# Optimization experiments

Hardware: AMD Instinct MI355X
Metric: run time of the kernel (lower is better)

Reference implementation:

```python
import jax, jax.numpy as jnp
import numpy as np

T, H, F = 4096, 4096, 14336

def setup_inputs() -> dict:
    key = jax.random.key(0)
    k1, k2, k3, k4 = jax.random.split(key, 4)
    s = 1.0 / np.sqrt(H)
    return {
        "x": jax.random.normal(k1, (T, H), dtype=jnp.float32),
        "expert_w1": jax.random.normal(k2, (H, F), dtype=jnp.float32) * s,
        "expert_v1": jax.random.normal(k3, (H, F), dtype=jnp.float32) * s,
        "expert_w2": jax.random.normal(k4, (H, F), dtype=jnp.float32) * s,
    }

def reference(x, expert_w1, expert_v1, expert_w2):
    # SwiGLU expert FFN: silu(x @ w1) * (x @ v1) @ w2.T
    gate_proj = jax.nn.silu(x @ expert_w1)          # [T, F]
    up_proj = x @ expert_v1                          # [T, F]
    down_proj = (gate_proj * up_proj) @ expert_w2.T  # [T, H]
    return down_proj
```

## Files before the change

### kernel.cpp

```cpp
#include <hip/hip_runtime.h>
#include <hip/hip_bf16.h>
#include <stdint.h>

#define TT 4096
#define HH 4096
#define FF 14336
#define NCAT (2 * FF)

typedef __attribute__((ext_vector_type(8))) short bf16x8;
typedef __attribute__((ext_vector_type(4))) float f32x4;

__device__ __forceinline__ unsigned short f32_to_bf16(float f) {
    union { float f; unsigned int u; } v; v.f = f;
    unsigned int r = v.u + 0x7FFFu + ((v.u >> 16) & 1u);
    return (unsigned short)(r >> 16);
}

#define GLOAD16(g, l)                                                          \
    __builtin_amdgcn_global_load_lds(                                          \
        (const __attribute__((address_space(1))) void*)(g),                    \
        (__attribute__((address_space(3))) void*)(l), 16, 0, 0)

__global__ void cvt_lin(const float* __restrict__ in,
                        unsigned short* __restrict__ out, long n4) {
    long stride = (long)gridDim.x * blockDim.x;
    for (long i = (long)blockIdx.x * blockDim.x + threadIdx.x; i < n4; i += stride) {
        float4 v = *(const float4*)(in + i * 4);
        ushort4 o;
        o.x = f32_to_bf16(v.x); o.y = f32_to_bf16(v.y);
        o.z = f32_to_bf16(v.z); o.w = f32_to_bf16(v.w);
        *(ushort4*)(out + i * 4) = o;
    }
}

__global__ void cvt_tri(const float* __restrict__ in,
                        unsigned short* __restrict__ out, int off) {
    __shared__ float tile[64][65];
    int bh = blockIdx.x & 63;
    int bf = blockIdx.x >> 6;
    int t = threadIdx.x;
    int r16 = t >> 4;
    int c4 = (t & 15) * 4;
#pragma unroll
    for (int it = 0; it < 4; ++it) {
        int h = r16 + it * 16;
        float4 v = *(const float4*)(in + (size_t)(bh * 64 + h) * FF + bf * 64 + c4);
        tile[h][c4 + 0] = v.x; tile[h][c4 + 1] = v.y;
        tile[h][c4 + 2] = v.z; tile[h][c4 + 3] = v.w;
    }
    __syncthreads();
#pragma unroll
    for (int it = 0; it < 4; ++it) {
        int f = r16 + it * 16;
        int fg = bf * 64 + f;
        int row_out = ((fg >> 4) << 5) + (fg & 15) + off;
        ushort4 o;
        o.x = f32_to_bf16(tile[c4 + 0][f]);
        o.y = f32_to_bf16(tile[c4 + 1][f]);
        o.z = f32_to_bf16(tile[c4 + 2][f]);
        o.w = f32_to_bf16(tile[c4 + 3][f]);
        *(ushort4*)(out + (size_t)row_out * HH + bh * 64 + c4) = o;
    }
}


#define STG_A(BUF, SLOT, T) do {                                               \
    char* d_ = (char*)smem + (((BUF)*2 + (SLOT)) << 14) + tid * 16;            \
    GLOAD16(Abase + ((size_t)oA[SLOT] + (size_t)(T) * 128), d_);               \
    GLOAD16(Abase + ((size_t)oA[SLOT] + CA + (size_t)(T) * 128), d_ + 8192);   \
  } while (0)

#define STG_B(BUF, SLOT, T) do {                                               \
    char* d_ = (char*)smem + 65536 + (((BUF)*2 + (SLOT)) << 14) + tid * 16;    \
    GLOAD16(Bbase + ((size_t)oB[SLOT] + (size_t)(T) * 128), d_);               \
    GLOAD16(Bbase + ((size_t)oB[SLOT] + CB + (size_t)(T) * 128), d_ + 8192);   \
  } while (0)

#define READ_A(DST, BUF, MQ) do {                                              \
    const char* pA_ = (const char*)smem + (((BUF)*2 + (MQ)) << 14);            \
    _Pragma("unroll") for (int i_ = 0; i_ < 4; ++i_)                           \
    _Pragma("unroll") for (int k_ = 0; k_ < 2; ++k_)                           \
      DST[i_][k_] = *(const bf16x8*)(pA_ + ((((wr*64 + i_*16 + fr) << 7) + k_*64 + kg2) ^ lmask)); \
  } while (0)

#define READ_B(DST, BUF, NQ) do {                                              \
    const char* pB_ = (const char*)smem + 65536 + (((BUF)*2 + (NQ)) << 14);    \
    _Pragma("unroll") for (int j_ = 0; j_ < 2; ++j_)                           \
    _Pragma("unroll") for (int k_ = 0; k_ < 2; ++k_)                           \
      DST[j_][k_] = *(const bf16x8*)(pB_ + ((((wc*32 + j_*16 + fr) << 7) + k_*64 + kg2) ^ lmask)); \
  } while (0)

#define MFMA_Q(MQ, NQ, AF, BF)                                                 \
    _Pragma("unroll") for (int i_ = 0; i_ < 4; ++i_)                           \
    _Pragma("unroll") for (int j_ = 0; j_ < 2; ++j_)                           \
    _Pragma("unroll") for (int k_ = 0; k_ < 2; ++k_)                           \
      acc[MQ][i_][NQ][j_] = __builtin_amdgcn_mfma_f32_16x16x32_bf16(           \
          AF[i_][k_], BF[j_][k_], acc[MQ][i_][NQ][j_], 0, 0, 0)

#define BAR do {                                                               \
    asm volatile("" ::: "memory");                                             \
    __builtin_amdgcn_s_barrier();                                              \
    asm volatile("" ::: "memory");                                             \
  } while (0)

#define VMC8 asm volatile("s_waitcnt vmcnt(8)" ::: "memory")
#define VMC0 asm volatile("s_waitcnt vmcnt(0)" ::: "memory")

#define PHX(READS, STAGES, MQ, NQ, AF, BF, FENCE, POST) do {                   \
    READS;                                                                     \
    STAGES;                                                                    \
    __builtin_amdgcn_s_setprio(1);                                             \
    MFMA_Q(MQ, NQ, AF, BF);                                                    \
    __builtin_amdgcn_s_setprio(0);                                             \
    FENCE;                                                                     \
    POST;                                                                      \
    BAR;                                                                       \
  } while (0)

#define PH(READS, STAGES, MQ, NQ, AF, BF, FENCE)                               \
    PHX(READS, STAGES, MQ, NQ, AF, BF, FENCE, )

#define HALF_STG(BUF, OB, TS)                                                  \
    PH(READ_A(af, BUF, 0), , 0, 0, af, bfA, );                                 \
    PH(READ_B(bfB, BUF, 1), STG_A(BUF, 0, TS); STG_B(BUF, 0, TS), 0, 1, af, bfB, ); \
    PH(READ_A(af, BUF, 1), STG_B(BUF, 1, TS), 1, 1, af, bfB, );                \
    PHX(, STG_A(BUF, 1, TS), 1, 0, af, bfA, VMC8, READ_B(bfA, OB, 0));

#define HALF_T1(BUF, OB)                                                       \
    PH(READ_A(af, BUF, 0), , 0, 0, af, bfA, );                                 \
    PH(READ_B(bfB, BUF, 1), , 0, 1, af, bfB, );                                \
    PH(READ_A(af, BUF, 1), , 1, 1, af, bfB, );                                 \
    PHX(, , 1, 0, af, bfA, VMC0, READ_B(bfA, OB, 0));

#define HALF_T2(BUF)                                                           \
    PH(READ_A(af, BUF, 0), , 0, 0, af, bfA, );                                 \
    PH(READ_B(bfB, BUF, 1), , 0, 1, af, bfB, );                                \
    PH(READ_A(af, BUF, 1), , 1, 1, af, bfB, );                                 \
    PHX(, , 1, 0, af, bfA, , );

#define GEMM8_CORE(A_, LDA_, B_, LDB_, NT_)                                    \
  extern __shared__ char smem[];                                               \
  const char* const Abase = (const char*)(A_);                                 \
  const char* const Bbase = (const char*)(B_);                                 \
  const size_t CA = (size_t)(LDA_) * 256;                                      \
  const size_t CB = (size_t)(LDB_) * 256;                                      \
  const int tid = threadIdx.x;                                                 \
  const int lane = tid & 63;                                                   \
  const int wid = tid >> 6;                                                    \
  const int wr = wid >> 2;                                                     \
  const int wc = wid & 3;                                                      \
  const int fr = lane & 15;                                                    \
  const int kg2 = ((lane >> 4) & 3) << 4;                                      \
  const int lmask = (fr & 6) << 4;                                             \
  f32x4 acc[2][4][2][2];                                                       \
  _Pragma("unroll") for (int a_ = 0; a_ < 2; ++a_)                             \
  _Pragma("unroll") for (int b_ = 0; b_ < 4; ++b_)                             \
  _Pragma("unroll") for (int c_ = 0; c_ < 2; ++c_)                             \
  _Pragma("unroll") for (int d_ = 0; d_ < 2; ++d_)                             \
    acc[a_][b_][c_][d_] = (f32x4){0.f, 0.f, 0.f, 0.f};                         \
  bf16x8 af[4][2], bfA[2][2], bfB[2][2];                                       \
  unsigned int oA[2], oB[2];                                                   \
  {                                                                            \
    int d_ = tid * 16;                                                         \
    int p_ = d_ ^ (((d_ >> 8) & 3) << 5);                                      \
    int prow = p_ >> 7, pcol = (p_ & 127) >> 1;                                \
    _Pragma("unroll") for (int s_ = 0; s_ < 2; ++s_) {                         \
      int grA = m0 + s_ * 64 + (prow & 63);                                    \
      oA[s_] = (unsigned)((size_t)grA * (LDA_) + pcol) * 2u;                   \
      int grB = n0 + (prow >> 5) * 64 + s_ * 32 + (prow & 31);                 \
      oB[s_] = (unsigned)((size_t)grB * (LDB_) + pcol) * 2u;                   \
    }                                                                          \
  }                                                                            \
     \
  STG_A(0, 0, 0); STG_B(0, 0, 0); STG_B(0, 1, 0); STG_A(0, 1, 0);              \
  STG_A(1, 0, 1); STG_B(1, 0, 1); STG_B(1, 1, 1); STG_A(1, 1, 1);              \
  VMC8;                                                                        \
  __builtin_amdgcn_s_barrier();                                                \
  asm volatile("" ::: "memory");                                               \
  READ_B(bfA, 0, 0);                                                           \
  const int niter = (NT_) / 2;                                                 \
  for (int I = 0; I < niter - 1; ++I) {                                        \
    HALF_STG(0, 1, 2 * I + 2)                                                  \
    HALF_STG(1, 0, 2 * I + 3)                                                  \
  }                                                                            \
  HALF_T1(0, 1)                                                                \
  HALF_T2(1)

__global__ __launch_bounds__(512)
__attribute__((amdgpu_waves_per_eu(1, 2))) void gemm_swiglu(
    const unsigned short* __restrict__ Xb,
    const unsigned short* __restrict__ Wcat,
    unsigned short* __restrict__ Act) {
    int lid = blockIdx.x;
    const int m0 = (lid & 15) * 256;
    const int n0 = (lid >> 4) * 256;

    GEMM8_CORE(Xb, HH, Wcat, HH, HH / 64)

    const int dm = ((lane >> 4) & 3) * 4;
    const int dn = lane & 15;
#pragma unroll
    for (int mq = 0; mq < 2; ++mq)
#pragma unroll
        for (int i = 0; i < 4; ++i)
#pragma unroll
            for (int nq = 0; nq < 2; ++nq) {
                int rowb = m0 + wr * 128 + mq * 64 + i * 16 + dm;
                int col = (n0 + wc * 64 + nq * 32) / 2 + dn;
                f32x4 g4 = acc[mq][i][nq][0];
                f32x4 u4 = acc[mq][i][nq][1];
#pragma unroll
                for (int r = 0; r < 4; ++r) {
                    float g = g4[r], u = u4[r];
                    float s = g * u / (1.0f + __expf(-g));
                    Act[(size_t)(rowb + r) * FF + col] = f32_to_bf16(s);
                }
            }
}

__global__ __launch_bounds__(512)
__attribute__((amdgpu_waves_per_eu(1, 2))) void gemm_down(
    const unsigned short* __restrict__ Act,
    const unsigned short* __restrict__ W2b,
    float* __restrict__ Out) {
    int lid = blockIdx.x;
    const int m0 = (lid & 15) * 256;
    const int n0 = (lid >> 4) * 256;

    GEMM8_CORE(Act, FF, W2b, FF, FF / 64)

    const int dm = ((lane >> 4) & 3) * 4;
    const int dn = lane & 15;
#pragma unroll
    for (int mq = 0; mq < 2; ++mq)
#pragma unroll
        for (int i = 0; i < 4; ++i)
#pragma unroll
            for (int nq = 0; nq < 2; ++nq)
#pragma unroll
                for (int j = 0; j < 2; ++j) {
                    int rowb = m0 + wr * 128 + mq * 64 + i * 16 + dm;
                    int col = n0 + wc * 64 + nq * 32 + j * 16 + dn;
                    f32x4 v = acc[mq][i][nq][j];
#pragma unroll
                    for (int r = 0; r < 4; ++r)
                        Out[(size_t)(rowb + r) * HH + col] = v[r];
                }
}

extern "C" void kernel_launch(void* const* d_in, const int* in_sizes, int n_in,
                              void* d_out, int out_size, void* d_ws, size_t ws_size,
                              hipStream_t stream) {
    const float* x  = (const float*)d_in[0];
    const float* w1 = (const float*)d_in[1];
    const float* v1 = (const float*)d_in[2];
    const float* w2 = (const float*)d_in[3];
    float* out = (float*)d_out;

    unsigned short* xb   = (unsigned short*)d_ws;
    unsigned short* wcat = xb + (size_t)TT * HH;
    unsigned short* w2b  = wcat + (size_t)NCAT * HH;
    unsigned short* act  = w2b + (size_t)HH * FF;

    hipFuncSetAttribute((const void*)gemm_swiglu,
                        hipFuncAttributeMaxDynamicSharedMemorySize, 131072);
    hipFuncSetAttribute((const void*)gemm_down,
                        hipFuncAttributeMaxDynamicSharedMemorySize, 131072);

    cvt_lin<<<2048, 256, 0, stream>>>(x, xb, (long)TT * HH / 4);
    cvt_lin<<<2048, 256, 0, stream>>>(w2, w2b, (long)HH * FF / 4);
    cvt_tri<<<(HH / 64) * (FF / 64), 256, 0, stream>>>(w1, wcat, 0);
    cvt_tri<<<(HH / 64) * (FF / 64), 256, 0, stream>>>(v1, wcat, 16);

    gemm_swiglu<<<(TT / 256) * (NCAT / 256), 512, 131072, stream>>>(xb, wcat, act);
    gemm_down<<<(TT / 256) * (HH / 256), 512, 131072, stream>>>(act, w2b, out);
}
```

Baseline: 1.283 ms.

## Restructure GEMM main loop into two-phase k-steps with shifted staging

Replaces the four-phase-per-half pipeline, which had one barrier per quarter MFMA block, with a two-phase k-step. Each phase reads a larger set of LDS fragments, issues global-to-LDS stages for future tiles, then runs two MFMA quadrants before a single barrier. This halves the number of barriers per k-tile and reshuffles when the A/B stages for the next buffers are issued (the A second half is staged one tile ahead into the other buffer), so the prologue wait becomes vmcnt(6). It aims to cut sync overhead, but it risks LDS write/read hazards and less even overlap between loads and MFMA.

New measurement: 1.302 ms. Within noise of the previous version (+1.5%).

```diff
diff --git a/kernel.cpp b/kernel.cpp
--- a/kernel.cpp
+++ b/kernel.cpp
@@ -104,39 +104,58 @@
   } while (0)
 
 #define VMC8 asm volatile("s_waitcnt vmcnt(8)" ::: "memory")
+#define VMC6 asm volatile("s_waitcnt vmcnt(6)" ::: "memory")
 #define VMC0 asm volatile("s_waitcnt vmcnt(0)" ::: "memory")
 
-#define PHX(READS, STAGES, MQ, NQ, AF, BF, FENCE, POST) do {                   \
-    READS;                                                                     \
-    STAGES;                                                                    \
-    __builtin_amdgcn_s_setprio(1);                                             \
-    MFMA_Q(MQ, NQ, AF, BF);                                                    \
-    __builtin_amdgcn_s_setprio(0);                                             \
-    FENCE;                                                                     \
-    POST;                                                                      \
+#define KSTEP(BUF, OB, TAU)                                                    \
+    READ_A(af, BUF, 0);                                                        \
+    READ_B(bfA, BUF, 0);                                                       \
+    READ_B(bfB, BUF, 1);                                                       \
+    STG_A(OB, 1, (TAU) + 1);                                                   \
+    __builtin_amdgcn_s_setprio(1);                                             \
+    MFMA_Q(0, 0, af, bfA);                                                     \
+    MFMA_Q(0, 1, af, bfB);                                                     \
+    __builtin_amdgcn_s_setprio(0);                                             \
+    VMC8;                                                                      \
     BAR;                                                                       \
-  } while (0)
-
-#define PH(READS, STAGES, MQ, NQ, AF, BF, FENCE)                               \
-    PHX(READS, STAGES, MQ, NQ, AF, BF, FENCE, )
-
-#define HALF_STG(BUF, OB, TS)                                                  \
-    PH(READ_A(af, BUF, 0), , 0, 0, af, bfA, );                                 \
-    PH(READ_B(bfB, BUF, 1), STG_A(BUF, 0, TS); STG_B(BUF, 0, TS), 0, 1, af, bfB, ); \
-    PH(READ_A(af, BUF, 1), STG_B(BUF, 1, TS), 1, 1, af, bfB, );                \
-    PHX(, STG_A(BUF, 1, TS), 1, 0, af, bfA, VMC8, READ_B(bfA, OB, 0));
-
-#define HALF_T1(BUF, OB)                                                       \
-    PH(READ_A(af, BUF, 0), , 0, 0, af, bfA, );                                 \
-    PH(READ_B(bfB, BUF, 1), , 0, 1, af, bfB, );                                \
-    PH(READ_A(af, BUF, 1), , 1, 1, af, bfB, );                                 \
-    PHX(, , 1, 0, af, bfA, VMC0, READ_B(bfA, OB, 0));
-
-#define HALF_T2(BUF)                                                           \
-    PH(READ_A(af, BUF, 0), , 0, 0, af, bfA, );                                 \
-    PH(READ_B(bfB, BUF, 1), , 0, 1, af, bfB, );                                \
-    PH(READ_A(af, BUF, 1), , 1, 1, af, bfB, );                                 \
-    PHX(, , 1, 0, af, bfA, , );
+    READ_A(af, BUF, 1);                                                        \
+    STG_A(BUF, 0, (TAU) + 2); STG_B(BUF, 0, (TAU) + 2); STG_B(BUF, 1, (TAU) + 2); \
+    __builtin_amdgcn_s_setprio(1);                                             \
+    MFMA_Q(1, 1, af, bfB);                                                     \
+    MFMA_Q(1, 0, af, bfA);                                                     \
+    __builtin_amdgcn_s_setprio(0);                                             \
+    VMC8;                                                                      \
+    BAR;
+
+#define KSTEP_T1(BUF, OB, TAU)                                                 \
+    READ_A(af, BUF, 0);                                                        \
+    READ_B(bfA, BUF, 0);                                                       \
+    READ_B(bfB, BUF, 1);                                                       \
+    STG_A(OB, 1, (TAU) + 1);                                                   \
+    __builtin_amdgcn_s_setprio(1);                                             \
+    MFMA_Q(0, 0, af, bfA);                                                     \
+    MFMA_Q(0, 1, af, bfB);                                                     \
+    __builtin_amdgcn_s_setprio(0);                                             \
+    VMC8;                                                                      \
+    BAR;                                                                       \
+    READ_A(af, BUF, 1);                                                        \
+    __builtin_amdgcn_s_setprio(1);                                             \
+    MFMA_Q(1, 1, af, bfB);                                                     \
+    MFMA_Q(1, 0, af, bfA);                                                     \
+    __builtin_amdgcn_s_setprio(0);                                             \
+    VMC0;                                                                      \
+    BAR;
+
+#define KSTEP_T2(BUF)                                                          \
+    READ_A(af, BUF, 0);                                                        \
+    READ_B(bfA, BUF, 0);                                                       \
+    READ_B(bfB, BUF, 1);                                                       \
+    MFMA_Q(0, 0, af, bfA);                                                     \
+    MFMA_Q(0, 1, af, bfB);                                                     \
+    BAR;                                                                       \
+    READ_A(af, BUF, 1);                                                        \
+    MFMA_Q(1, 1, af, bfB);                                                     \
+    MFMA_Q(1, 0, af, bfA);
 
 #define GEMM8_CORE(A_, LDA_, B_, LDB_, NT_)                                    \
   extern __shared__ char smem[];                                               \
@@ -171,20 +190,20 @@
       oB[s_] = (unsigned)((size_t)grB * (LDB_) + pcol) * 2u;                   \
     }                                                                          \
   }                                                                            \
-     \
+      \
+       \
   STG_A(0, 0, 0); STG_B(0, 0, 0); STG_B(0, 1, 0); STG_A(0, 1, 0);              \
-  STG_A(1, 0, 1); STG_B(1, 0, 1); STG_B(1, 1, 1); STG_A(1, 1, 1);              \
-  VMC8;                                                                        \
+  STG_A(1, 0, 1); STG_B(1, 0, 1); STG_B(1, 1, 1);                              \
+  VMC6;                                                                        \
   __builtin_amdgcn_s_barrier();                                                \
   asm volatile("" ::: "memory");                                               \
-  READ_B(bfA, 0, 0);                                                           \
   const int niter = (NT_) / 2;                                                 \
   for (int I = 0; I < niter - 1; ++I) {                                        \
-    HALF_STG(0, 1, 2 * I + 2)                                                  \
-    HALF_STG(1, 0, 2 * I + 3)                                                  \
+    KSTEP(0, 1, 2 * I)                                                         \
+    KSTEP(1, 0, 2 * I + 1)                                                     \
   }                                                                            \
-  HALF_T1(0, 1)                                                                \
-  HALF_T2(1)
+  KSTEP_T1(0, 1, (NT_) - 2)                                                    \
+  KSTEP_T2(1)
 
 __global__ __launch_bounds__(512)
 __attribute__((amdgpu_waves_per_eu(1, 2))) void gemm_swiglu(
```
